# Kernel optimization log

Hardware: AMD Instinct MI355X
Metric: run time of the kernel (lower is better)

Reference implementation:

```python
import jax, jax.numpy as jnp
import numpy as np

IN_DIM = 128
HID = 128
NUM_CLASSES = 10
N_NODES = 100000
N_EDGES = 1600000
NUM_GRAPHS = 128


def setup_inputs() -> dict:
    key = jax.random.key(0)
    ks = jax.random.split(key, 12)
    X = jax.random.normal(ks[0], (N_NODES, IN_DIM), dtype=jnp.float32)
    EI = jax.random.randint(ks[1], (2, N_EDGES), 0, N_NODES, dtype=jnp.int64)
    batch = jnp.sort(jax.random.randint(ks[2], (N_NODES,), 0, NUM_GRAPHS, dtype=jnp.int64))
    s_in = 1.0 / np.sqrt(IN_DIM)
    s_h = 1.0 / np.sqrt(HID)
    s_m = 1.0 / np.sqrt(2 * HID)
    params = {
        'W1': jax.random.uniform(ks[3], (IN_DIM, HID), jnp.float32, -s_in, s_in),
        'b1': jnp.zeros((HID,), jnp.float32),
        'W2': jax.random.uniform(ks[4], (HID, HID), jnp.float32, -s_h, s_h),
        'b2': jnp.zeros((HID,), jnp.float32),
        'W3': jax.random.uniform(ks[5], (HID, HID), jnp.float32, -s_h, s_h),
        'b3': jnp.zeros((HID,), jnp.float32),
        'Wm1': jax.random.uniform(ks[6], (2 * HID, HID), jnp.float32, -s_m, s_m),
        'bm1': jnp.zeros((HID,), jnp.float32),
        'Wm2': jax.random.uniform(ks[7], (HID, NUM_CLASSES), jnp.float32, -s_h, s_h),
        'bm2': jnp.zeros((NUM_CLASSES,), jnp.float32),
    }
    return dict(X=X, EI=EI, batch=batch, num_graphs=NUM_GRAPHS, **params)


def _gcn_norm(EI, n):
    # add self loops, compute D^{-1/2}[row] * D^{-1/2}[col]
    loops = jnp.arange(n, dtype=EI.dtype)
    row = jnp.concatenate([EI[0], loops])
    col = jnp.concatenate([EI[1], loops])
    deg = jax.ops.segment_sum(jnp.ones_like(row, dtype=jnp.float32), row, num_segments=n)
    dis = (deg + 1e-12) ** -0.5
    norm = dis[row] * dis[col]
    return row, col, norm


def _gcn_layer(x, row, col, norm, W, b):
    h = x @ W + b                       # [N, out]
    msg = h[col] * norm[:, None]        # gather + scale  [E+N, out]
    return jax.ops.segment_sum(msg, row, num_segments=x.shape[0])  # scatter-add


def _pool_mean_max(x, batch, num_graphs):
    s = jax.ops.segment_sum(x, batch, num_segments=num_graphs)
    cnt = jax.ops.segment_sum(jnp.ones((x.shape[0],), x.dtype), batch, num_segments=num_graphs)
    mean = s / (cnt[:, None] + 1e-12)
    mx = jax.ops.segment_max(x, batch, num_segments=num_graphs)
    return jnp.concatenate([mean, mx], axis=1)


def reference(X, EI, batch, num_graphs, W1, b1, W2, b2, W3, b3, Wm1, bm1, Wm2, bm2):
    n = X.shape[0]
    row, col, norm = _gcn_norm(EI, n)
    x = jax.nn.relu(_gcn_layer(X, row, col, norm, W1, b1))
    x = jax.nn.relu(_gcn_layer(x, row, col, norm, W2, b2))
    x = jax.nn.relu(_gcn_layer(x, row, col, norm, W3, b3))
    g = _pool_mean_max(x, batch, num_graphs)
    h = jax.nn.relu(g @ Wm1 + bm1)
    return h @ Wm2 + bm2
```

## Files before the change

### kernel.cpp

```cpp
#include <hip/hip_runtime.h>
#include <hip/hip_fp16.h>
#include <cstdint>
#include <cstddef>

#define DIM 128
#define NG 128
#define NCLS 10
#define PSLICE 8
#define CPAD 64
#define NOWN 256
#define RPB 391
#define NPBLK 1024
#define OCAP 16
#define OVCAP 65536

typedef _Float16 f16;
typedef __attribute__((ext_vector_type(8))) _Float16 f16x8;
typedef __attribute__((ext_vector_type(4))) float f32x4;


__global__ __launch_bounds__(256) void k_part(
    const int* __restrict__ rw, const int* __restrict__ cl, int E,
    unsigned* __restrict__ buckets, int* __restrict__ bcnt,
    unsigned long long* __restrict__ ovf, int* __restrict__ ovfn) {
  __shared__ int lcnt[NOWN];
  if (threadIdx.x < NOWN) lcnt[threadIdx.x] = 0;
  __syncthreads();
  int b = blockIdx.x;
  int C = (E + NPBLK - 1) / NPBLK;
  int s = b * C;
  int e = s + C;
  if (e > E) e = E;
  for (int i = s + (int)threadIdx.x; i < e; i += 256) {
    int r = rw[i], c = cl[i];
    int o = (unsigned)r / RPB;
    int li = r - o * RPB;
    int sl = atomicAdd(&lcnt[o], 1);
    if (sl < OCAP) {
      buckets[((size_t)o * NPBLK + b) * OCAP + sl] =
          ((unsigned)li << 17) | (unsigned)c;
    } else {
      int oi = atomicAdd(ovfn, 1);
      if (oi < OVCAP)
        ovf[oi] = ((unsigned long long)(unsigned)r << 32) | (unsigned)c;
    }
  }
  __syncthreads();
  if (threadIdx.x < NOWN) {
    int v = lcnt[threadIdx.x];
    bcnt[threadIdx.x * NPBLK + b] = v < OCAP ? v : OCAP;
  }
}

__global__ __launch_bounds__(256) void k_place(
    const unsigned* __restrict__ buckets, const int* __restrict__ bcnt,
    const unsigned long long* __restrict__ ovf, const int* __restrict__ ovfn,
    int* __restrict__ cnt, float* __restrict__ dis, int* __restrict__ csrc,
    int N) {
  extern __shared__ int sm[];
  int* lcnt = sm;
  int* csr = sm + ((RPB + 3) & ~3);
  int o = blockIdx.x;
  int r0 = o * RPB;
  int rows = N - r0;
  if (rows > RPB) rows = RPB;
  if (rows <= 0) return;
  for (int i = threadIdx.x; i < rows; i += 256) lcnt[i] = 0;
  __syncthreads();
  const int* bc = bcnt + o * NPBLK;
  const unsigned* bp = buckets + (size_t)o * NPBLK * OCAP;
  for (int j = (int)threadIdx.x; j < NPBLK * OCAP; j += 256) {
    int seg = j >> 4;
    int pos = j & 15;
    if (pos < bc[seg]) {
      unsigned ent = bp[j];
      int li = (int)(ent >> 17);
      int c = (int)(ent & 0x1ffffu);
      int sl = atomicAdd(&lcnt[li], 1);
      if (sl < CPAD) csr[(li << 6) + sl] = c;
    }
  }
  int nov = *ovfn;
  if (nov > OVCAP) nov = OVCAP;
  for (int j = (int)threadIdx.x; j < nov; j += 256) {
    unsigned long long ent = ovf[j];
    int r = (int)(unsigned)(ent >> 32);
    int li = r - r0;
    if (li >= 0 && li < rows) {
      int c = (int)(unsigned)(ent & 0xffffffffu);
      int sl = atomicAdd(&lcnt[li], 1);
      if (sl < CPAD) csr[(li << 6) + sl] = c;
    }
  }
  __syncthreads();
  uint4* dst = (uint4*)(csrc + ((size_t)r0 << 6));
  const uint4* src = (const uint4*)csr;
  int n4 = rows * 16;
  for (int j = (int)threadIdx.x; j < n4; j += 256) dst[j] = src[j];
  for (int i = threadIdx.x; i < rows; i += 256) {
    int v = lcnt[i];
    cnt[r0 + i] = v;
    dis[r0 + i] = rsqrtf((float)(v + 1));
  }
}

__global__ void k_wt(const float* __restrict__ W1, const float* __restrict__ W2,
                     const float* __restrict__ W3, __half* __restrict__ Wt1,
                     __half* __restrict__ Wt2, __half* __restrict__ Wt3) {
  int gi = blockIdx.x * 256 + threadIdx.x;
  int m = gi / (DIM * DIM);
  int i = gi % (DIM * DIM);
  const float* W = (m == 0) ? W1 : (m == 1) ? W2 : W3;
  __half* Wt = (m == 0) ? Wt1 : (m == 1) ? Wt2 : Wt3;
  int k = i >> 7, c = i & 127;
  Wt[(size_t)c * DIM + k] = __float2half(W[(size_t)k * DIM + c]);
}


template <int FP32IN>
__global__ __launch_bounds__(256, 3) void k_gemm(
    const void* __restrict__ Ain, const __half* __restrict__ Wt,
    const float* __restrict__ bias, const float* __restrict__ dis,
    __half* __restrict__ Hh, int N) {
  int t = threadIdx.x;
  int lane = t & 63;
  int wv = t >> 6;
  int l15 = lane & 15, lg = lane >> 4;
  int cb = (wv & 1) * 64;

  f16x8 bfr[4][4];
#pragma unroll
  for (int ct = 0; ct < 4; ++ct) {
    int c = cb + ct * 16 + l15;
    const f16* wp = (const f16*)Wt + (size_t)c * DIM + lg * 8;
#pragma unroll
    for (int ks = 0; ks < 4; ++ks) bfr[ks][ct] = *(const f16x8*)(wp + ks * 32);
  }
  float bv[4];
#pragma unroll
  for (int ct = 0; ct < 4; ++ct) bv[ct] = bias[cb + ct * 16 + l15];

  const int nt2 = (N + 31) / 32;
  for (int t2 = blockIdx.x; t2 < nt2; t2 += gridDim.x) {
    int row0 = t2 * 32 + (wv >> 1) * 16;
    int rA = row0 + l15;
    if (rA > N - 1) rA = N - 1;
    f16x8 afr[4];
    if constexpr (FP32IN) {
      const float* ap = (const float*)Ain + (size_t)rA * DIM + lg * 8;
#pragma unroll
      for (int ks = 0; ks < 4; ++ks) {
        float4 v0 = *(const float4*)(ap + ks * 32);
        float4 v1 = *(const float4*)(ap + ks * 32 + 4);
        f16x8 a;
        a[0] = (f16)v0.x; a[1] = (f16)v0.y; a[2] = (f16)v0.z; a[3] = (f16)v0.w;
        a[4] = (f16)v1.x; a[5] = (f16)v1.y; a[6] = (f16)v1.z; a[7] = (f16)v1.w;
        afr[ks] = a;
      }
    } else {
      const f16* ap = (const f16*)Ain + (size_t)rA * DIM + lg * 8;
#pragma unroll
      for (int ks = 0; ks < 4; ++ks) afr[ks] = *(const f16x8*)(ap + ks * 32);
    }

    f32x4 acc[4];
#pragma unroll
    for (int ct = 0; ct < 4; ++ct) acc[ct] = (f32x4){0.f, 0.f, 0.f, 0.f};
#pragma unroll
    for (int ks = 0; ks < 4; ++ks)
#pragma unroll
      for (int ct = 0; ct < 4; ++ct)
        acc[ct] = __builtin_amdgcn_mfma_f32_16x16x32_f16(afr[ks], bfr[ks][ct], acc[ct], 0, 0, 0);

#pragma unroll
    for (int j = 0; j < 4; ++j) {
      int r = row0 + lg * 4 + j;
      if (r < N) {
        float dr = dis[r];
#pragma unroll
        for (int ct = 0; ct < 4; ++ct) {
          float o = (acc[ct][j] + bv[ct]) * dr;
          Hh[(size_t)r * DIM + cb + ct * 16 + l15] = __float2half(o);
        }
      }
    }
  }
}


__global__ __launch_bounds__(256) void k_agg(
    const __half* __restrict__ Hh, __half* __restrict__ Ah,
    const int* __restrict__ csrc, const int* __restrict__ cntA,
    const float* __restrict__ dis, int N) {
  int wave = (int)(((size_t)blockIdx.x * blockDim.x + threadIdx.x) >> 6);
  int lane = threadIdx.x & 63;
  int g = lane >> 4;
  int q = lane & 15;
  int r = wave * 4 + g;
  if (r >= N) return;
  int cnt = cntA[r];
  if (cnt > CPAD) cnt = CPAD;
  float dr = dis[r];
  const int* cp = csrc + ((size_t)r << 6);
  const f16* hb = (const f16*)Hh + q * 8;

  float4 aA0 = {0,0,0,0}, aA1 = {0,0,0,0};
  float4 aB0 = {0,0,0,0}, aB1 = {0,0,0,0};
  float4 aC0 = {0,0,0,0}, aC1 = {0,0,0,0};
  float4 aD0 = {0,0,0,0}, aD1 = {0,0,0,0};

#define ACC8(u, x0, x1)                                                   \
  {                                                                       \
    float2 f_;                                                            \
    f_ = __half22float2(*reinterpret_cast<const __half2*>(&(u).x));       \
    x0.x += f_.x; x0.y += f_.y;                                           \
    f_ = __half22float2(*reinterpret_cast<const __half2*>(&(u).y));       \
    x0.z += f_.x; x0.w += f_.y;                                           \
    f_ = __half22float2(*reinterpret_cast<const __half2*>(&(u).z));       \
    x1.x += f_.x; x1.y += f_.y;                                           \
    f_ = __half22float2(*reinterpret_cast<const __half2*>(&(u).w));       \
    x1.z += f_.x; x1.w += f_.y;                                           \
  }

  int i = 0;
  for (; i + 3 < cnt; i += 4) {
    int c0 = cp[i], c1 = cp[i + 1], c2 = cp[i + 2], c3 = cp[i + 3];
    uint4 u0 = *(const uint4*)(hb + (size_t)c0 * DIM);
    uint4 u1 = *(const uint4*)(hb + (size_t)c1 * DIM);
    uint4 u2 = *(const uint4*)(hb + (size_t)c2 * DIM);
    uint4 u3 = *(const uint4*)(hb + (size_t)c3 * DIM);
    ACC8(u0, aA0, aA1);
    ACC8(u1, aB0, aB1);
    ACC8(u2, aC0, aC1);
    ACC8(u3, aD0, aD1);
  }
  for (; i < cnt; ++i) {
    int c0 = cp[i];
    uint4 u0 = *(const uint4*)(hb + (size_t)c0 * DIM);
    ACC8(u0, aA0, aA1);
  }
  {
    uint4 us = *(const uint4*)(hb + (size_t)r * DIM);
    ACC8(us, aA0, aA1);
  }
#undef ACC8
  float4 s0, s1;
  s0.x = (aA0.x + aB0.x) + (aC0.x + aD0.x);
  s0.y = (aA0.y + aB0.y) + (aC0.y + aD0.y);
  s0.z = (aA0.z + aB0.z) + (aC0.z + aD0.z);
  s0.w = (aA0.w + aB0.w) + (aC0.w + aD0.w);
  s1.x = (aA1.x + aB1.x) + (aC1.x + aD1.x);
  s1.y = (aA1.y + aB1.y) + (aC1.y + aD1.y);
  s1.z = (aA1.z + aB1.z) + (aC1.z + aD1.z);
  s1.w = (aA1.w + aB1.w) + (aC1.w + aD1.w);
  float o0 = fmaxf(dr * s0.x, 0.f), o1 = fmaxf(dr * s0.y, 0.f);
  float o2 = fmaxf(dr * s0.z, 0.f), o3 = fmaxf(dr * s0.w, 0.f);
  float o4 = fmaxf(dr * s1.x, 0.f), o5 = fmaxf(dr * s1.y, 0.f);
  float o6 = fmaxf(dr * s1.z, 0.f), o7 = fmaxf(dr * s1.w, 0.f);
  __half2 p0 = __floats2half2_rn(o0, o1);
  __half2 p1 = __floats2half2_rn(o2, o3);
  __half2 p2 = __floats2half2_rn(o4, o5);
  __half2 p3 = __floats2half2_rn(o6, o7);
  uint4 u;
  u.x = *(unsigned int*)&p0;
  u.y = *(unsigned int*)&p1;
  u.z = *(unsigned int*)&p2;
  u.w = *(unsigned int*)&p3;
  *(uint4*)((f16*)Ah + (size_t)r * DIM + q * 8) = u;
}


__global__ void k_bounds(const int* __restrict__ batch, int N, int G,
                         int* __restrict__ starts) {
  int i = blockIdx.x * blockDim.x + threadIdx.x;
  if (i >= N) return;
  int b = batch[i];
  int pb = (i == 0) ? -1 : batch[i - 1];
  for (int g = pb + 1; g <= b; ++g) starts[g] = i;
  if (i == N - 1) {
    for (int g = b + 1; g <= G; ++g) starts[g] = N;
  }
}

__global__ void k_pool1(const __half* __restrict__ A, const int* __restrict__ starts,
                        float* __restrict__ part) {
  int g = blockIdx.x / PSLICE, sl = blockIdx.x % PSLICE;
  int c = threadIdx.x;
  int s = starts[g], e = starts[g + 1];
  int len = e - s;
  int ns = s + (len * sl) / PSLICE;
  int ne = s + (len * (sl + 1)) / PSLICE;
  float sum = 0.f, mx = -INFINITY;
  for (int n = ns; n < ne; ++n) {
    float v = __half2float(A[(size_t)n * DIM + c]);
    sum += v;
    mx = fmaxf(mx, v);
  }
  part[((size_t)(g * PSLICE + sl) * 2 + 0) * DIM + c] = sum;
  part[((size_t)(g * PSLICE + sl) * 2 + 1) * DIM + c] = mx;
}

__global__ void k_pool2(const float* __restrict__ part, const int* __restrict__ starts,
                        float* __restrict__ GF) {
  int g = blockIdx.x;
  int c = threadIdx.x;
  float sum = 0.f, mx = -INFINITY;
  for (int sl = 0; sl < PSLICE; ++sl) {
    sum += part[((size_t)(g * PSLICE + sl) * 2 + 0) * DIM + c];
    mx = fmaxf(mx, part[((size_t)(g * PSLICE + sl) * 2 + 1) * DIM + c]);
  }
  int cntg = starts[g + 1] - starts[g];
  GF[(size_t)g * 256 + c] = sum / ((float)cntg + 1e-12f);
  GF[(size_t)g * 256 + 128 + c] = mx;
}


__global__ void k_mlp1(const float* __restrict__ GF, const float* __restrict__ Wm1,
                       const float* __restrict__ bm1, float* __restrict__ H1) {
  __shared__ float gs[256];
  int g = blockIdx.x, j = threadIdx.x;
  gs[j] = GF[(size_t)g * 256 + j];
  gs[j + 128] = GF[(size_t)g * 256 + 128 + j];
  __syncthreads();
  float acc = bm1[j];
#pragma unroll 8
  for (int k = 0; k < 256; ++k) acc = fmaf(gs[k], Wm1[k * DIM + j], acc);
  H1[(size_t)g * DIM + j] = fmaxf(acc, 0.f);
}

__global__ void k_mlp2(const float* __restrict__ H1, const float* __restrict__ Wm2,
                       const float* __restrict__ bm2, float* __restrict__ out) {
  __shared__ float hs[DIM];
  int g = blockIdx.x, j = threadIdx.x;
  hs[j] = H1[(size_t)g * DIM + j];
  hs[j + 64] = H1[(size_t)g * DIM + j + 64];
  __syncthreads();
  if (j < NCLS) {
    float acc = bm2[j];
#pragma unroll 8
    for (int k = 0; k < DIM; ++k) acc = fmaf(hs[k], Wm2[k * NCLS + j], acc);
    out[(size_t)g * NCLS + j] = acc;
  }
}


static inline size_t al256(size_t x) { return (x + 255) & ~(size_t)255; }

extern "C" void kernel_launch(void* const* d_in, const int* in_sizes, int n_in,
                              void* d_out, int out_size, void* d_ws, size_t ws_size,
                              hipStream_t stream) {
  const float* X = (const float*)d_in[0];
  const int* EI = (const int*)d_in[1];
  const int* batch = (const int*)d_in[2];
  const float* W1 = (const float*)d_in[4];
  const float* b1 = (const float*)d_in[5];
  const float* W2 = (const float*)d_in[6];
  const float* b2 = (const float*)d_in[7];
  const float* W3 = (const float*)d_in[8];
  const float* b3 = (const float*)d_in[9];
  const float* Wm1 = (const float*)d_in[10];
  const float* bm1 = (const float*)d_in[11];
  const float* Wm2 = (const float*)d_in[12];
  const float* bm2 = (const float*)d_in[13];
  float* OUT = (float*)d_out;

  const int N = in_sizes[0] / DIM;
  const int E = in_sizes[1] / 2;
  const int G = NG;

  const int* EI_row = EI;
  const int* EI_col = EI + E;

  char* p = (char*)d_ws;
  size_t off = 0;
  auto take = [&](size_t bytes) { void* r = p + off; off = al256(off + bytes); return r; };

  int* cnt = (int*)take((size_t)N * 4);
  int* bcnt = (int*)take((size_t)NOWN * NPBLK * 4);
  int* ovfn = (int*)take(256);
  unsigned long long* ovf = (unsigned long long*)take((size_t)OVCAP * 8);
  int* starts = (int*)take((size_t)(G + 1) * 4);
  float* dis = (float*)take((size_t)N * 4);
  int* csrc = (int*)take((size_t)N * CPAD * 4);
  unsigned* buckets = (unsigned*)take((size_t)NOWN * NPBLK * OCAP * 4);
  __half* Hh = (__half*)take((size_t)N * DIM * 2);
  __half* Ah = (__half*)take((size_t)N * DIM * 2);
  __half* Wt1 = (__half*)take((size_t)DIM * DIM * 2);
  __half* Wt2 = (__half*)take((size_t)DIM * DIM * 2);
  __half* Wt3 = (__half*)take((size_t)DIM * DIM * 2);
  float* part = (float*)take((size_t)G * PSLICE * 2 * DIM * 4);
  float* GF = (float*)take((size_t)G * 256 * 4);
  float* H1 = (float*)take((size_t)G * DIM * 4);
  (void)ws_size; (void)n_in; (void)out_size;

  hipMemsetAsync(ovfn, 0, 4, stream);

  k_part<<<NPBLK, 256, 0, stream>>>(EI_row, EI_col, E, buckets, bcnt, ovf, ovfn);
  const int placeLds = ((RPB + 3) & ~3) * 4 + RPB * 64 * 4;
  k_place<<<NOWN, 256, placeLds, stream>>>(buckets, bcnt, ovf, ovfn, cnt, dis, csrc, N);
  k_wt<<<192, 256, 0, stream>>>(W1, W2, W3, Wt1, Wt2, Wt3);

  const int aggBlocks = (N * 16 + 255) / 256;

  k_gemm<1><<<512, 256, 0, stream>>>(X, Wt1, b1, dis, Hh, N);
  k_agg<<<aggBlocks, 256, 0, stream>>>(Hh, Ah, csrc, cnt, dis, N);
  k_gemm<0><<<512, 256, 0, stream>>>(Ah, Wt2, b2, dis, Hh, N);
  k_agg<<<aggBlocks, 256, 0, stream>>>(Hh, Ah, csrc, cnt, dis, N);
  k_gemm<0><<<512, 256, 0, stream>>>(Ah, Wt3, b3, dis, Hh, N);
  k_agg<<<aggBlocks, 256, 0, stream>>>(Hh, Ah, csrc, cnt, dis, N);

  k_bounds<<<(N + 255) / 256, 256, 0, stream>>>(batch, N, G, starts);
  k_pool1<<<G * PSLICE, DIM, 0, stream>>>(Ah, starts, part);
  k_pool2<<<G, DIM, 0, stream>>>(part, starts, GF);

  k_mlp1<<<G, DIM, 0, stream>>>(GF, Wm1, bm1, H1);
  k_mlp2<<<G, 64, 0, stream>>>(H1, Wm2, bm2, OUT);
}
```

Baseline: 367.7 us.

## Vectorize edge partition loads, fuse pooling tail and MLP head, double GEMM grid

The edge partition kernel now reads row and column indices as int4 vectors, and the per-block chunk size is rounded up to a multiple of four. The separate bounds kernel is removed; graph segment starts are now found by binary search over the sorted batch array inside the pooling kernels. The pool reduction and both MLP layers are merged into one head kernel, which drops three launches and two intermediate buffers. The GEMM grid size goes from 512 to 1024 blocks. In exchange, every block repeats the binary search, and the int4 loads assume 16-byte alignment of each chunk start and of the column array base (which sits E ints after the row array).

New measurement: 369.3 us. Within noise of the previous version (+0.4%).

```diff
diff --git a/kernel.cpp b/kernel.cpp
--- a/kernel.cpp
+++ b/kernel.cpp
@@ -27,12 +27,11 @@
   if (threadIdx.x < NOWN) lcnt[threadIdx.x] = 0;
   __syncthreads();
   int b = blockIdx.x;
-  int C = (E + NPBLK - 1) / NPBLK;
+  int C = (((E + NPBLK - 1) / NPBLK + 3) & ~3);
   int s = b * C;
   int e = s + C;
   if (e > E) e = E;
-  for (int i = s + (int)threadIdx.x; i < e; i += 256) {
-    int r = rw[i], c = cl[i];
+  auto put = [&](int r, int c) {
     int o = (unsigned)r / RPB;
     int li = r - o * RPB;
     int sl = atomicAdd(&lcnt[o], 1);
@@ -43,6 +42,18 @@
       int oi = atomicAdd(ovfn, 1);
       if (oi < OVCAP)
         ovf[oi] = ((unsigned long long)(unsigned)r << 32) | (unsigned)c;
+    }
+  };
+  for (int i = s + (int)threadIdx.x * 4; i < e; i += 1024) {
+    if (i + 3 < e) {
+      int4 r4 = *(const int4*)(rw + i);
+      int4 c4 = *(const int4*)(cl + i);
+      put(r4.x, c4.x);
+      put(r4.y, c4.y);
+      put(r4.z, c4.z);
+      put(r4.w, c4.w);
+    } else {
+      for (int j = i; j < e; ++j) put(rw[j], cl[j]);
     }
   }
   __syncthreads();
@@ -270,23 +281,21 @@
 }
 
 
-__global__ void k_bounds(const int* __restrict__ batch, int N, int G,
-                         int* __restrict__ starts) {
-  int i = blockIdx.x * blockDim.x + threadIdx.x;
-  if (i >= N) return;
-  int b = batch[i];
-  int pb = (i == 0) ? -1 : batch[i - 1];
-  for (int g = pb + 1; g <= b; ++g) starts[g] = i;
-  if (i == N - 1) {
-    for (int g = b + 1; g <= G; ++g) starts[g] = N;
-  }
-}
-
-__global__ void k_pool1(const __half* __restrict__ A, const int* __restrict__ starts,
-                        float* __restrict__ part) {
+__device__ __forceinline__ int lower_bound_batch(const int* batch, int N, int g) {
+  int lo = 0, hi = N;
+  while (lo < hi) {
+    int mid = (lo + hi) >> 1;
+    if (batch[mid] < g) lo = mid + 1; else hi = mid;
+  }
+  return lo;
+}
+
+__global__ void k_pool1(const __half* __restrict__ A, const int* __restrict__ batch,
+                        int N, float* __restrict__ part) {
   int g = blockIdx.x / PSLICE, sl = blockIdx.x % PSLICE;
   int c = threadIdx.x;
-  int s = starts[g], e = starts[g + 1];
+  int s = lower_bound_batch(batch, N, g);
+  int e = lower_bound_batch(batch, N, g + 1);
   int len = e - s;
   int ns = s + (len * sl) / PSLICE;
   int ne = s + (len * (sl + 1)) / PSLICE;
@@ -300,8 +309,12 @@
   part[((size_t)(g * PSLICE + sl) * 2 + 1) * DIM + c] = mx;
 }
 
-__global__ void k_pool2(const float* __restrict__ part, const int* __restrict__ starts,
-                        float* __restrict__ GF) {
+__global__ void k_head(const float* __restrict__ part, const int* __restrict__ batch,
+                       int N, const float* __restrict__ Wm1,
+                       const float* __restrict__ bm1, const float* __restrict__ Wm2,
+                       const float* __restrict__ bm2, float* __restrict__ out) {
+  __shared__ float gs[256];
+  __shared__ float hs[DIM];
   int g = blockIdx.x;
   int c = threadIdx.x;
   float sum = 0.f, mx = -INFINITY;
@@ -309,37 +322,21 @@
     sum += part[((size_t)(g * PSLICE + sl) * 2 + 0) * DIM + c];
     mx = fmaxf(mx, part[((size_t)(g * PSLICE + sl) * 2 + 1) * DIM + c]);
   }
-  int cntg = starts[g + 1] - starts[g];
-  GF[(size_t)g * 256 + c] = sum / ((float)cntg + 1e-12f);
-  GF[(size_t)g * 256 + 128 + c] = mx;
-}
-
-
-__global__ void k_mlp1(const float* __restrict__ GF, const float* __restrict__ Wm1,
-                       const float* __restrict__ bm1, float* __restrict__ H1) {
-  __shared__ float gs[256];
-  int g = blockIdx.x, j = threadIdx.x;
-  gs[j] = GF[(size_t)g * 256 + j];
-  gs[j + 128] = GF[(size_t)g * 256 + 128 + j];
-  __syncthreads();
-  float acc = bm1[j];
+  int s = lower_bound_batch(batch, N, g);
+  int e = lower_bound_batch(batch, N, g + 1);
+  gs[c] = sum / ((float)(e - s) + 1e-12f);
+  gs[c + 128] = mx;
+  __syncthreads();
+  float acc = bm1[c];
 #pragma unroll 8
-  for (int k = 0; k < 256; ++k) acc = fmaf(gs[k], Wm1[k * DIM + j], acc);
-  H1[(size_t)g * DIM + j] = fmaxf(acc, 0.f);
-}
-
-__global__ void k_mlp2(const float* __restrict__ H1, const float* __restrict__ Wm2,
-                       const float* __restrict__ bm2, float* __restrict__ out) {
-  __shared__ float hs[DIM];
-  int g = blockIdx.x, j = threadIdx.x;
-  hs[j] = H1[(size_t)g * DIM + j];
-  hs[j + 64] = H1[(size_t)g * DIM + j + 64];
-  __syncthreads();
-  if (j < NCLS) {
-    float acc = bm2[j];
+  for (int k = 0; k < 256; ++k) acc = fmaf(gs[k], Wm1[k * DIM + c], acc);
+  hs[c] = fmaxf(acc, 0.f);
+  __syncthreads();
+  if (c < NCLS) {
+    float a2 = bm2[c];
 #pragma unroll 8
-    for (int k = 0; k < DIM; ++k) acc = fmaf(hs[k], Wm2[k * NCLS + j], acc);
-    out[(size_t)g * NCLS + j] = acc;
+    for (int k = 0; k < DIM; ++k) a2 = fmaf(hs[k], Wm2[k * NCLS + c], a2);
+    out[(size_t)g * NCLS + c] = a2;
   }
 }
 
@@ -379,7 +376,6 @@
   int* bcnt = (int*)take((size_t)NOWN * NPBLK * 4);
   int* ovfn = (int*)take(256);
   unsigned long long* ovf = (unsigned long long*)take((size_t)OVCAP * 8);
-  int* starts = (int*)take((size_t)(G + 1) * 4);
   float* dis = (float*)take((size_t)N * 4);
   int* csrc = (int*)take((size_t)N * CPAD * 4);
   unsigned* buckets = (unsigned*)take((size_t)NOWN * NPBLK * OCAP * 4);
@@ -389,8 +385,6 @@
   __half* Wt2 = (__half*)take((size_t)DIM * DIM * 2);
   __half* Wt3 = (__half*)take((size_t)DIM * DIM * 2);
   float* part = (float*)take((size_t)G * PSLICE * 2 * DIM * 4);
-  float* GF = (float*)take((size_t)G * 256 * 4);
-  float* H1 = (float*)take((size_t)G * DIM * 4);
   (void)ws_size; (void)n_in; (void)out_size;
 
   hipMemsetAsync(ovfn, 0, 4, stream);
@@ -402,17 +396,13 @@
 
   const int aggBlocks = (N * 16 + 255) / 256;
 
-  k_gemm<1><<<512, 256, 0, stream>>>(X, Wt1, b1, dis, Hh, N);
+  k_gemm<1><<<1024, 256, 0, stream>>>(X, Wt1, b1, dis, Hh, N);
   k_agg<<<aggBlocks, 256, 0, stream>>>(Hh, Ah, csrc, cnt, dis, N);
-  k_gemm<0><<<512, 256, 0, stream>>>(Ah, Wt2, b2, dis, Hh, N);
+  k_gemm<0><<<1024, 256, 0, stream>>>(Ah, Wt2, b2, dis, Hh, N);
   k_agg<<<aggBlocks, 256, 0, stream>>>(Hh, Ah, csrc, cnt, dis, N);
-  k_gemm<0><<<512, 256, 0, stream>>>(Ah, Wt3, b3, dis, Hh, N);
+  k_gemm<0><<<1024, 256, 0, stream>>>(Ah, Wt3, b3, dis, Hh, N);
   k_agg<<<aggBlocks, 256, 0, stream>>>(Hh, Ah, csrc, cnt, dis, N);
 
-  k_bounds<<<(N + 255) / 256, 256, 0, stream>>>(batch, N, G, starts);
-  k_pool1<<<G * PSLICE, DIM, 0, stream>>>(Ah, starts, part);
-  k_pool2<<<G, DIM, 0, stream>>>(part, starts, GF);
-
-  k_mlp1<<<G, DIM, 0, stream>>>(GF, Wm1, bm1, H1);
-  k_mlp2<<<G, 64, 0, stream>>>(H1, Wm2, bm2, OUT);
-}
+  k_pool1<<<G * PSLICE, DIM, 0, stream>>>(Ah, batch, N, part);
+  k_head<<<G, DIM, 0, stream>>>(part, batch, N, Wm1, bm1, Wm2, bm2, OUT);
+}
```
